# Kernel optimization log

Measured on AMD Instinct MI355X. Metric: run time of the kernel, lower is better.

## Reference

```python
import jax, jax.numpy as jnp
import numpy as np

BLOCK = 128
FP8_MAX = 448.0


def _quantize_weight_blockwise(w):
    """Blockwise fp8 quantization of weight [O, I] -> (fp8-valued f32 weight, [O/B, I/B] scales)."""
    O, I = w.shape
    wb = w.reshape(O // BLOCK, BLOCK, I // BLOCK, BLOCK)
    amax = jnp.maximum(jnp.max(jnp.abs(wb), axis=(1, 3), keepdims=True), 1e-12)
    scale = amax / FP8_MAX  # [O/B,1,I/B,1]
    w_fp8 = (wb / scale).astype(jnp.float8_e4m3fn).astype(jnp.float32).reshape(O, I)
    return w_fp8, scale[:, 0, :, 0]


def setup_inputs() -> dict:
    key = jax.random.key(0)
    k1, k2 = jax.random.split(key)
    tokens, input_size, output_size = 8192, 4096, 4096
    x = jax.random.normal(k1, (tokens, input_size), dtype=jnp.float32)
    w_hp = jax.random.normal(k2, (output_size, input_size), dtype=jnp.float32) * 0.02
    weight, weight_scale_inv = _quantize_weight_blockwise(w_hp)
    return {"x": x, "weight": weight, "weight_scale_inv": weight_scale_inv}


def reference(x, weight, weight_scale_inv):
    # --- dynamic per-token fp8 quantization of activations ---
    amax = jnp.maximum(jnp.max(jnp.abs(x), axis=-1, keepdims=True), 1e-12)  # [T,1]
    x_scale = amax / FP8_MAX                                                # [T,1] f32
    x_fp8 = (x / x_scale).astype(jnp.float8_e4m3fn).astype(jnp.float32)     # fp8-valued f32
    # --- blockwise dequant of fp8 weight with weight_scale_inv ---
    O, I = weight.shape
    scale_full = jnp.repeat(jnp.repeat(weight_scale_inv, BLOCK, axis=0), BLOCK, axis=1)  # [O,I]
    w_deq = weight * scale_full
    # --- fp8 block-scaled GEMM (dequantized-equivalent math) ---
    y = jnp.einsum('tk,ok->to', x_fp8, w_deq) * x_scale  # [T, O]
    return y
```

## Files before the change

kernel.cpp:

```cpp
#include <hip/hip_runtime.h>
#include <stdint.h>

#define FP8_MAX 448.0f
#define TOKENS  8192
#define IDIM    4096
#define ODIM    4096

typedef float f32x4 __attribute__((ext_vector_type(4)));
typedef int   i32x4 __attribute__((ext_vector_type(4)));
typedef int   i32x8 __attribute__((ext_vector_type(8)));

__device__ __forceinline__ void async_copy16(const uint8_t* g, uint8_t* l) {
  __builtin_amdgcn_global_load_lds((const __attribute__((address_space(1))) void*)g,
                                   (__attribute__((address_space(3))) void*)l,
                                   16, 0, 0);
}

__global__ __launch_bounds__(256) void prep_kernel(
    const float* __restrict__ x, const float* __restrict__ w,
    uint8_t* __restrict__ xq, uint8_t* __restrict__ wq, float* __restrict__ xsc) {
  const int tid = threadIdx.x;
  if (blockIdx.x < TOKENS) {
    const int row = blockIdx.x;
    const f32x4* xr = (const f32x4*)(x + (size_t)row * IDIM);

    f32x4 v[4];
    float amax = 0.0f;
    #pragma unroll
    for (int k = 0; k < 4; k++) {
      v[k] = xr[tid + k * 256];
      amax = fmaxf(amax, fmaxf(fmaxf(fabsf(v[k].x), fabsf(v[k].y)),
                               fmaxf(fabsf(v[k].z), fabsf(v[k].w))));
    }
    #pragma unroll
    for (int off = 32; off > 0; off >>= 1)
      amax = fmaxf(amax, __shfl_xor(amax, off, 64));

    __shared__ float smax[4];
    if ((tid & 63) == 0) smax[tid >> 6] = amax;
    __syncthreads();
    amax = fmaxf(fmaxf(smax[0], smax[1]), fmaxf(smax[2], smax[3]));
    amax = fmaxf(amax, 1e-12f);
    const float scale = amax / FP8_MAX;
    if (tid == 0) xsc[row] = scale;

    uint32_t* out = (uint32_t*)(xq + (size_t)row * IDIM);
    #pragma unroll
    for (int k = 0; k < 4; k++) {
      float a = v[k].x / scale, b = v[k].y / scale;
      float c = v[k].z / scale, d = v[k].w / scale;
      int p = __builtin_amdgcn_cvt_pk_fp8_f32(a, b, 0, false);
      p = __builtin_amdgcn_cvt_pk_fp8_f32(c, d, p, true);
      out[tid + k * 256] = (uint32_t)p;
    }
  } else {
    const size_t base = (size_t)(blockIdx.x - TOKENS) * 4096;
    const f32x4* wp = (const f32x4*)(w + base);
    uint32_t* out = (uint32_t*)(wq + base);
    #pragma unroll
    for (int k = 0; k < 4; k++) {
      f32x4 v = wp[tid + k * 256];
      int p = __builtin_amdgcn_cvt_pk_fp8_f32(v.x, v.y, 0, false);
      p = __builtin_amdgcn_cvt_pk_fp8_f32(v.z, v.w, p, true);
      out[tid + k * 256] = (uint32_t)p;
    }
  }
}

__global__ __launch_bounds__(256) void gemm_fp8_kernel(
    const uint8_t* __restrict__ xq, const uint8_t* __restrict__ wq,
    const float* __restrict__ xsc, const float* __restrict__ wsi,
    float* __restrict__ y) {
  __shared__ __align__(16) uint8_t As[128 * 128];
  __shared__ __align__(16) uint8_t Bs[128 * 128];

  const int tid  = threadIdx.x;
  const int bo   = blockIdx.x & 31;
  const int bt   = blockIdx.x >> 5;
  const int t0   = bt << 7;
  const int o0   = bo << 7;
  const int lane = tid & 63;
  const int wave = tid >> 6;
  const int wr   = (wave >> 1) << 6;
  const int wc   = (wave & 1) << 6;
  const int ln   = lane & 15;
  const int quad = lane >> 4;

  const int rb  = tid >> 3;
  const int cs  = ((tid & 7) ^ (rb & 7)) << 4;
  const int lds = tid << 4;

  const int c0 = quad << 1;
  int aoff[4][2], boff[4][2];
  #pragma unroll
  for (int i = 0; i < 4; i++) {
    const int ra = wr + i * 16 + ln;
    const int sa = ra & 7;
    aoff[i][0] = ra * 128 + ((c0 ^ sa) << 4);
    aoff[i][1] = ra * 128 + (((c0 + 1) ^ sa) << 4);
    const int rb2 = wc + i * 16 + ln;
    const int sb = rb2 & 7;
    boff[i][0] = rb2 * 128 + ((c0 ^ sb) << 4);
    boff[i][1] = rb2 * 128 + (((c0 + 1) ^ sb) << 4);
  }

  f32x4 outer[4][4];
  #pragma unroll
  for (int i = 0; i < 4; i++)
    #pragma unroll
    for (int j = 0; j < 4; j++)
      outer[i][j] = (f32x4)(0.0f);

  const float* wsrow = wsi + bo * 32;
  const int ident = 0x7f7f7f7f;
  const f32x4 zero4 = (f32x4)(0.0f);

  for (int kb = 0; kb < 32; kb++) {
    const int k0 = kb << 7;
    #pragma unroll
    for (int u = 0; u < 4; u++) {
      async_copy16(xq + ((size_t)(t0 + u * 32 + rb) << 12) + (k0 + cs),
                   As + u * 4096 + lds);
      async_copy16(wq + ((size_t)(o0 + u * 32 + rb) << 12) + (k0 + cs),
                   Bs + u * 4096 + lds);
    }
    __syncthreads();

    i32x8 a[4], b[4];
    #pragma unroll
    for (int i = 0; i < 4; i++) {
      i32x4 lo = *(const i32x4*)(As + aoff[i][0]);
      i32x4 hi = *(const i32x4*)(As + aoff[i][1]);
      a[i] = __builtin_shufflevector(lo, hi, 0, 1, 2, 3, 4, 5, 6, 7);
    }
    #pragma unroll
    for (int j = 0; j < 4; j++) {
      i32x4 lo = *(const i32x4*)(Bs + boff[j][0]);
      i32x4 hi = *(const i32x4*)(Bs + boff[j][1]);
      b[j] = __builtin_shufflevector(lo, hi, 0, 1, 2, 3, 4, 5, 6, 7);
    }

    const float s = wsrow[kb];
    #pragma unroll
    for (int i = 0; i < 4; i++)
      #pragma unroll
      for (int j = 0; j < 4; j++) {
        f32x4 t = __builtin_amdgcn_mfma_scale_f32_16x16x128_f8f6f4(
            a[i], b[j], zero4, 0, 0, 0, ident, 0, ident);
        outer[i][j] += s * t;
      }
    __syncthreads();
  }

  #pragma unroll
  for (int i = 0; i < 4; i++) {
    #pragma unroll
    for (int r = 0; r < 4; r++) {
      const int t = t0 + wr + i * 16 + quad * 4 + r;
      const float sc = xsc[t];
      float* yp = y + ((size_t)t << 12) + o0 + wc + ln;
      #pragma unroll
      for (int j = 0; j < 4; j++)
        yp[j * 16] = outer[i][j][r] * sc;
    }
  }
}

extern "C" void kernel_launch(void* const* d_in, const int* in_sizes, int n_in,
                              void* d_out, int out_size, void* d_ws, size_t ws_size,
                              hipStream_t stream) {
  const float* x   = (const float*)d_in[0];
  const float* w   = (const float*)d_in[1];
  const float* wsi = (const float*)d_in[2];
  float* y = (float*)d_out;

  uint8_t* xq = (uint8_t*)d_ws;
  uint8_t* wq = xq + (size_t)TOKENS * IDIM;
  float*  xsc = (float*)(wq + (size_t)ODIM * IDIM);

  prep_kernel<<<TOKENS + ((size_t)ODIM * IDIM) / 4096, 256, 0, stream>>>(x, w, xq, wq, xsc);
  gemm_fp8_kernel<<<(TOKENS / 128) * (ODIM / 128), 256, 0, stream>>>(xq, wq, xsc, wsi, y);
}
```

Before: 423.8 us.

## Double-buffer LDS tiles in fp8 GEMM, remap blocks, use wave-per-row prep

The GEMM now ping-pongs between two LDS buffers, issuing async global-to-LDS loads for the next K block while MFMAs run on the current one, so there is one barrier per step instead of two. Block indices are permuted across groups of 8 to change which tiles run concurrently, aiming for better L2 reuse. The prep kernel assigns one wave per row, which removes the shared-memory reduction and barrier. The second buffer doubles LDS use to 64KB per block and may lower occupancy; correctness also depends on global_load_lds completion being covered by the barrier waits.

```diff
diff --git a/kernel.cpp b/kernel.cpp
--- a/kernel.cpp
+++ b/kernel.cpp
@@ -19,50 +19,47 @@
 __global__ __launch_bounds__(256) void prep_kernel(
     const float* __restrict__ x, const float* __restrict__ w,
     uint8_t* __restrict__ xq, uint8_t* __restrict__ wq, float* __restrict__ xsc) {
-  const int tid = threadIdx.x;
-  if (blockIdx.x < TOKENS) {
-    const int row = blockIdx.x;
+  const int lane = threadIdx.x & 63;
+  const int wid  = threadIdx.x >> 6;
+
+  if (blockIdx.x < 2048) {
+    const int row = blockIdx.x * 4 + wid;
     const f32x4* xr = (const f32x4*)(x + (size_t)row * IDIM);
 
-    f32x4 v[4];
+    f32x4 v[16];
     float amax = 0.0f;
     #pragma unroll
-    for (int k = 0; k < 4; k++) {
-      v[k] = xr[tid + k * 256];
+    for (int k = 0; k < 16; k++) {
+      v[k] = xr[lane + k * 64];
       amax = fmaxf(amax, fmaxf(fmaxf(fabsf(v[k].x), fabsf(v[k].y)),
                                fmaxf(fabsf(v[k].z), fabsf(v[k].w))));
     }
     #pragma unroll
     for (int off = 32; off > 0; off >>= 1)
       amax = fmaxf(amax, __shfl_xor(amax, off, 64));
-
-    __shared__ float smax[4];
-    if ((tid & 63) == 0) smax[tid >> 6] = amax;
-    __syncthreads();
-    amax = fmaxf(fmaxf(smax[0], smax[1]), fmaxf(smax[2], smax[3]));
     amax = fmaxf(amax, 1e-12f);
     const float scale = amax / FP8_MAX;
-    if (tid == 0) xsc[row] = scale;
+    if (lane == 0) xsc[row] = scale;
 
     uint32_t* out = (uint32_t*)(xq + (size_t)row * IDIM);
     #pragma unroll
-    for (int k = 0; k < 4; k++) {
+    for (int k = 0; k < 16; k++) {
       float a = v[k].x / scale, b = v[k].y / scale;
       float c = v[k].z / scale, d = v[k].w / scale;
       int p = __builtin_amdgcn_cvt_pk_fp8_f32(a, b, 0, false);
       p = __builtin_amdgcn_cvt_pk_fp8_f32(c, d, p, true);
-      out[tid + k * 256] = (uint32_t)p;
+      out[lane + k * 64] = (uint32_t)p;
     }
   } else {
-    const size_t base = (size_t)(blockIdx.x - TOKENS) * 4096;
-    const f32x4* wp = (const f32x4*)(w + base);
-    uint32_t* out = (uint32_t*)(wq + base);
+    const int row = (blockIdx.x - 2048) * 4 + wid;
+    const f32x4* wp = (const f32x4*)(w + (size_t)row * IDIM);
+    uint32_t* out = (uint32_t*)(wq + (size_t)row * IDIM);
     #pragma unroll
-    for (int k = 0; k < 4; k++) {
-      f32x4 v = wp[tid + k * 256];
-      int p = __builtin_amdgcn_cvt_pk_fp8_f32(v.x, v.y, 0, false);
-      p = __builtin_amdgcn_cvt_pk_fp8_f32(v.z, v.w, p, true);
-      out[tid + k * 256] = (uint32_t)p;
+    for (int k = 0; k < 16; k++) {
+      f32x4 t = wp[lane + k * 64];
+      int p = __builtin_amdgcn_cvt_pk_fp8_f32(t.x, t.y, 0, false);
+      p = __builtin_amdgcn_cvt_pk_fp8_f32(t.z, t.w, p, true);
+      out[lane + k * 64] = (uint32_t)p;
     }
   }
 }
@@ -71,12 +68,15 @@
     const uint8_t* __restrict__ xq, const uint8_t* __restrict__ wq,
     const float* __restrict__ xsc, const float* __restrict__ wsi,
     float* __restrict__ y) {
-  __shared__ __align__(16) uint8_t As[128 * 128];
-  __shared__ __align__(16) uint8_t Bs[128 * 128];
+  __shared__ __align__(16) uint8_t As0[128 * 128];
+  __shared__ __align__(16) uint8_t Bs0[128 * 128];
+  __shared__ __align__(16) uint8_t As1[128 * 128];
+  __shared__ __align__(16) uint8_t Bs1[128 * 128];
 
   const int tid  = threadIdx.x;
-  const int bo   = blockIdx.x & 31;
-  const int bt   = blockIdx.x >> 5;
+  const int bid  = (blockIdx.x & 7) * 256 + (blockIdx.x >> 3);
+  const int bo   = bid & 31;
+  const int bt   = bid >> 5;
   const int t0   = bt << 7;
   const int o0   = bo << 7;
   const int lane = tid & 63;
@@ -115,32 +115,28 @@
   const int ident = 0x7f7f7f7f;
   const f32x4 zero4 = (f32x4)(0.0f);
 
-  for (int kb = 0; kb < 32; kb++) {
+  auto stage = [&](uint8_t* Ad, uint8_t* Bd, int kb) {
     const int k0 = kb << 7;
     #pragma unroll
     for (int u = 0; u < 4; u++) {
       async_copy16(xq + ((size_t)(t0 + u * 32 + rb) << 12) + (k0 + cs),
-                   As + u * 4096 + lds);
+                   Ad + u * 4096 + lds);
       async_copy16(wq + ((size_t)(o0 + u * 32 + rb) << 12) + (k0 + cs),
-                   Bs + u * 4096 + lds);
+                   Bd + u * 4096 + lds);
     }
-    __syncthreads();
+  };
 
+  auto compute = [&](const uint8_t* Ab, const uint8_t* Bb, float s) {
     i32x8 a[4], b[4];
     #pragma unroll
     for (int i = 0; i < 4; i++) {
-      i32x4 lo = *(const i32x4*)(As + aoff[i][0]);
-      i32x4 hi = *(const i32x4*)(As + aoff[i][1]);
-      a[i] = __builtin_shufflevector(lo, hi, 0, 1, 2, 3, 4, 5, 6, 7);
+      i32x4 alo = *(const i32x4*)(Ab + aoff[i][0]);
+      i32x4 ahi = *(const i32x4*)(Ab + aoff[i][1]);
+      a[i] = __builtin_shufflevector(alo, ahi, 0, 1, 2, 3, 4, 5, 6, 7);
+      i32x4 blo = *(const i32x4*)(Bb + boff[i][0]);
+      i32x4 bhi = *(const i32x4*)(Bb + boff[i][1]);
+      b[i] = __builtin_shufflevector(blo, bhi, 0, 1, 2, 3, 4, 5, 6, 7);
     }
-    #pragma unroll
-    for (int j = 0; j < 4; j++) {
-      i32x4 lo = *(const i32x4*)(Bs + boff[j][0]);
-      i32x4 hi = *(const i32x4*)(Bs + boff[j][1]);
-      b[j] = __builtin_shufflevector(lo, hi, 0, 1, 2, 3, 4, 5, 6, 7);
-    }
-
-    const float s = wsrow[kb];
     #pragma unroll
     for (int i = 0; i < 4; i++)
       #pragma unroll
@@ -149,6 +145,18 @@
             a[i], b[j], zero4, 0, 0, 0, ident, 0, ident);
         outer[i][j] += s * t;
       }
+  };
+
+  stage(As0, Bs0, 0);
+  __syncthreads();
+
+  for (int kb = 0; kb < 32; kb += 2) {
+    if (kb + 1 < 32) stage(As1, Bs1, kb + 1);
+    compute(As0, Bs0, wsrow[kb]);
+    __syncthreads();
+
+    if (kb + 2 < 32) stage(As0, Bs0, kb + 2);
+    compute(As1, Bs1, wsrow[kb + 1]);
     __syncthreads();
   }
 
@@ -178,6 +186,6 @@
   uint8_t* wq = xq + (size_t)TOKENS * IDIM;
   float*  xsc = (float*)(wq + (size_t)ODIM * IDIM);
 
-  prep_kernel<<<TOKENS + ((size_t)ODIM * IDIM) / 4096, 256, 0, stream>>>(x, w, xq, wq, xsc);
-  gemm_fp8_kernel<<<(TOKENS / 128) * (ODIM / 128), 256, 0, stream>>>(xq, wq, xsc, wsi, y);
+  prep_kernel<<<3072, 256, 0, stream>>>(x, w, xq, wq, xsc);
+  gemm_fp8_kernel<<<2048, 256, 0, stream>>>(xq, wq, xsc, wsi, y);
 }
```

Measured after the change: 452.0 us. 1.07x slower.
